# Kernel optimization log

Hardware: AMD Instinct MI355X
Metric: run time of the kernel (lower is better)

Reference implementation:

```python
import jax, jax.numpy as jnp
import numpy as np

UNITS = 512


def setup_inputs() -> dict:
    key = jax.random.key(0)
    ks = jax.random.split(key, 9)
    B, D, U = 16384, 512, UNITS
    return {
        "inputs": jax.random.normal(ks[0], (B, 2 * D), dtype=jnp.float32),
        "h": jax.random.normal(ks[1], (B, U), dtype=jnp.float32),
        "w_z": jax.random.normal(ks[2], (D, U), dtype=jnp.float32) * 0.05,
        "u_z": jax.random.normal(ks[3], (U, U), dtype=jnp.float32) * 0.05,
        "b_z": jnp.zeros((U,), dtype=jnp.float32),
        "w_r": jax.random.normal(ks[4], (D, U), dtype=jnp.float32) * 0.05,
        "u_r": jax.random.normal(ks[5], (U, U), dtype=jnp.float32) * 0.05,
        "b_r": jnp.zeros((U,), dtype=jnp.float32),
        "w_h": jax.random.normal(ks[6], (D, U), dtype=jnp.float32) * 0.05,
        "u_h": jax.random.normal(ks[7], (U, U), dtype=jnp.float32) * 0.05,
        "b_h": jnp.zeros((U,), dtype=jnp.float32),
    }


def reference(inputs, h, w_z, u_z, b_z, w_r, u_r, b_r, w_h, u_h, b_h):
    # Split concatenated (input, mask) halves along the feature axis.
    x, mask = jnp.split(inputs, 2, axis=1)  # each (B, D)
    # Faithful to source: mask @ zeros((D, U)) is identically zero.
    out_mask = jnp.matmul(mask, jnp.zeros((mask.shape[-1], UNITS), dtype=inputs.dtype))  # (B, U)
    h_masked = h * out_mask
    z_t = jax.nn.sigmoid(jnp.matmul(x, w_z) + jnp.matmul(h_masked, u_z) + b_z)
    r_t = jax.nn.sigmoid(jnp.matmul(x, w_r) + jnp.matmul(h_masked, u_r) + b_r)
    h_t = jnp.tanh(jnp.matmul(x, w_h) + jnp.matmul(r_t * h_masked, u_h) + b_h)
    h_t_seq = z_t * h_t + (1.0 - z_t) * h_masked  # (B, U)
    h_t_forward = jnp.concatenate((h_t_seq, out_mask), axis=1)  # (B, 2U)
    return (h_t_forward, h_t_seq)
```

## Files before the change

### kernel.cpp

```cpp
#include <hip/hip_runtime.h>

typedef __attribute__((ext_vector_type(4))) float f32x4;
typedef __attribute__((ext_vector_type(8))) short short8;
typedef __attribute__((ext_vector_type(8))) unsigned short ushort8;
typedef __attribute__((ext_vector_type(4))) unsigned short ushort4v;

#define M_ROWS 16384
#define KDIM 512
#define UDIM 512
#define IN_STRIDE 1024
#define NSTEP 16

__device__ __forceinline__ unsigned short f2bf(float f) {
    union { float f; unsigned u; } v; v.f = f;
    unsigned r = v.u + 0x7FFFu + ((v.u >> 16) & 1u);
    return (unsigned short)(r >> 16);
}

#define GLD16(g, l)                                                            \
    __builtin_amdgcn_global_load_lds(                                          \
        (const __attribute__((address_space(1))) void*)(g),                    \
        (__attribute__((address_space(3))) void*)(l), 16, 0, 0)

__global__ __launch_bounds__(256) void pack_w(
    const float* __restrict__ w_z,
    const float* __restrict__ w_h,
    unsigned short* __restrict__ Wp)
{
    int tid = blockIdx.x * 256 + threadIdx.x;
    int s   = tid & 511;
    int kt  = (tid >> 9) & 15;
    int ub  = tid >> 13;
    int jj  = s >> 2;
    int sl  = (s & 3) ^ ((jj >> 1) & 3);
    int k   = kt * 32 + sl * 8;
    const float* w = ((jj >> 5) & 1) ? w_h : w_z;
    int u = ub * 64 + ((jj >> 6) << 5) + (jj & 31);
    ushort8 v;
#pragma unroll
    for (int i = 0; i < 8; ++i)
        v[i] = f2bf(w[(size_t)(k + i) * UDIM + u]);
    *reinterpret_cast<ushort8*>(Wp + (size_t)tid * 8) = v;
}

__global__ __launch_bounds__(256, 3) void gru_gemm(
    const float* __restrict__ x,
    const unsigned short* __restrict__ Wp,
    const float* __restrict__ b_z,
    const float* __restrict__ b_h,
    float* __restrict__ out)
{
    __shared__ __align__(16) unsigned char smem[40960];
    unsigned short* shA = (unsigned short*)smem;
    unsigned short* shB = (unsigned short*)(smem + 16384);

    const int tid  = threadIdx.x;
    const int lane = tid & 63;
    const int wid  = tid >> 6;
    const int wm   = wid >> 1;
    const int wn   = wid & 1;

    const int d  = blockIdx.x;
    const int bx = (d >> 3) & 7;
    const int by = (d & 7) * 16 + (d >> 6);
    const int u0   = bx * 64;
    const int brow = by * 128;

    const int s0a = wid * 128 + lane;
    const int s1a = s0a + 64;
    const int r0 = s0a >> 2, r1 = s1a >> 2;
    const int sl0 = (s0a & 3) ^ ((r0 >> 1) & 3);
    const int sl1 = (s1a & 3) ^ ((r1 >> 1) & 3);
    const float* g0 = x + (size_t)(brow + r0) * IN_STRIDE + sl0 * 8;
    const float* g1 = x + (size_t)(brow + r1) * IN_STRIDE + sl1 * 8;

    const unsigned short* bp = Wp + (size_t)bx * 65536 + (size_t)s0a * 8;

    f32x4 acc[4][4];
#pragma unroll
    for (int m = 0; m < 4; ++m)
#pragma unroll
        for (int n = 0; n < 4; ++n)
            acc[m][n] = (f32x4){0.f, 0.f, 0.f, 0.f};

    f32x4 rA[2][4];

#define ISSUE_A(t, set)                                                        \
    {                                                                          \
        rA[set][0] = *reinterpret_cast<const f32x4*>(g0 + (t) * 32);           \
        rA[set][1] = *reinterpret_cast<const f32x4*>(g0 + (t) * 32 + 4);       \
        rA[set][2] = *reinterpret_cast<const f32x4*>(g1 + (t) * 32);           \
        rA[set][3] = *reinterpret_cast<const f32x4*>(g1 + (t) * 32 + 4);       \
    }

#define ISSUE_B(t, b)                                                          \
    {                                                                          \
        GLD16(bp + (size_t)(t) * 4096,       shB + (b) * 4096 + wid * 1024);   \
        GLD16(bp + (size_t)(t) * 4096 + 512, shB + (b) * 4096 + wid * 1024 + 512); \
    }

#define CVT_WRITE_A(set, b)                                                    \
    {                                                                          \
        ushort8 v0, v1;                                                        \
        _Pragma("unroll")                                                      \
        for (int i = 0; i < 4; ++i) { v0[i] = f2bf(rA[set][0][i]); v0[i+4] = f2bf(rA[set][1][i]); } \
        _Pragma("unroll")                                                      \
        for (int i = 0; i < 4; ++i) { v1[i] = f2bf(rA[set][2][i]); v1[i+4] = f2bf(rA[set][3][i]); } \
        *reinterpret_cast<ushort8*>(&shA[(b) * 4096 + s0a * 8]) = v0;          \
        *reinterpret_cast<ushort8*>(&shA[(b) * 4096 + s1a * 8]) = v1;          \
    }

    const int fr = lane & 15;
    const int ks = lane >> 4;
    const int xo = (fr >> 1) & 3;
    int aoff[4], boff[4];
#pragma unroll
    for (int m = 0; m < 4; ++m)
        aoff[m] = (wm * 64 + m * 16 + fr) * 32 + ((ks ^ xo) << 3);
#pragma unroll
    for (int n = 0; n < 4; ++n)
        boff[n] = (wn * 64 + n * 16 + fr) * 32 + ((ks ^ xo) << 3);

    ISSUE_A(0, 0); ISSUE_B(0, 0);
    ISSUE_A(1, 1); ISSUE_B(1, 1);
    asm volatile("s_waitcnt vmcnt(6)" ::: "memory");
    CVT_WRITE_A(0, 0);
    asm volatile("s_waitcnt lgkmcnt(0)" ::: "memory");
    asm volatile("s_barrier" ::: "memory");

#pragma unroll
    for (int t = 0; t < NSTEP; ++t) {
        if (t + 2 < NSTEP) {
            ISSUE_A(t + 2, (t + 2) & 1);
            ISSUE_B(t + 2, (t + 2) % 3);
        }
        const int ba = t & 1, bb = t % 3;
        short8 af[4], bfrag[4];
#pragma unroll
        for (int m = 0; m < 4; ++m)
            af[m] = *reinterpret_cast<const short8*>(&shA[ba * 4096 + aoff[m]]);
#pragma unroll
        for (int n = 0; n < 4; ++n)
            bfrag[n] = *reinterpret_cast<const short8*>(&shB[bb * 4096 + boff[n]]);
#pragma unroll
        for (int m = 0; m < 4; ++m)
#pragma unroll
            for (int n = 0; n < 4; ++n)
                acc[m][n] = __builtin_amdgcn_mfma_f32_16x16x32_bf16(af[m], bfrag[n], acc[m][n], 0, 0, 0);
        if (t + 1 < NSTEP) {
            if (t + 2 < NSTEP) {
                asm volatile("s_waitcnt vmcnt(6)" ::: "memory");
            } else {
                asm volatile("s_waitcnt vmcnt(0)" ::: "memory");
            }
            CVT_WRITE_A((t + 1) & 1, (t + 1) & 1);
            asm volatile("s_waitcnt lgkmcnt(0)" ::: "memory");
            asm volatile("s_barrier" ::: "memory");
        }
    }

    __syncthreads();

    float* plane = (float*)smem;
    const int fq = lane >> 4;
#pragma unroll
    for (int p = 0; p < 2; ++p) {
        int ucol = wn * 32 + p * 16 + fr;
        float bz = b_z[u0 + ucol];
        float bh = b_h[u0 + ucol];
#pragma unroll
        for (int m = 0; m < 4; ++m) {
            int row0 = wm * 64 + m * 16 + fq * 4;
            f32x4 az = acc[m][p];
            f32x4 ah = acc[m][p + 2];
#pragma unroll
            for (int j = 0; j < 4; ++j) {
                float zt = 1.f / (1.f + __expf(-(az[j] + bz)));
                float e  = __expf(2.f * (ah[j] + bh));
                float s  = zt * (1.f - 2.f / (e + 1.f));
                plane[(row0 + j) * 68 + ucol] = s;
            }
        }
    }
    __syncthreads();

    float* fwd = out;
    float* seq = out + (size_t)M_ROWS * 1024;
    const f32x4 z4 = (f32x4){0.f, 0.f, 0.f, 0.f};
    const int c4 = (tid & 15) * 4;
#pragma unroll
    for (int it = 0; it < 8; ++it) {
        int row = it * 16 + (tid >> 4);
        f32x4 v = *reinterpret_cast<const f32x4*>(&plane[row * 68 + c4]);
        size_t grow = (size_t)(brow + row);
        *reinterpret_cast<f32x4*>(&fwd[grow * 1024 + u0 + c4])       = v;
        *reinterpret_cast<f32x4*>(&fwd[grow * 1024 + 512 + u0 + c4]) = z4;
        *reinterpret_cast<f32x4*>(&seq[grow * 512 + u0 + c4])        = v;
    }
#undef ISSUE_A
#undef ISSUE_B
#undef CVT_WRITE_A
}

#define LDSS 40
__global__ __launch_bounds__(256) void gru_fused_legacy(
    const float* __restrict__ inp, const float* __restrict__ w_z,
    const float* __restrict__ b_z, const float* __restrict__ w_h,
    const float* __restrict__ b_h, float* __restrict__ out)
{
    __shared__ __align__(16) unsigned short Asl[2][128][LDSS];
    __shared__ __align__(16) unsigned short Bsl[2][128][LDSS];
    const int tid = threadIdx.x, lane = tid & 63, wid = tid >> 6;
    const int wm = wid >> 1, wn = wid & 1;
    const int u0 = blockIdx.x * 64, brow = blockIdx.y * 128;
    f32x4 acc[4][4];
#pragma unroll
    for (int m = 0; m < 4; ++m)
#pragma unroll
        for (int n = 0; n < 4; ++n) acc[m][n] = (f32x4){0.f,0.f,0.f,0.f};
    f32x4 rA[4], rB[4];
#define STAGE_LOAD(kt) { const int k0_=(kt)*32; \
    _Pragma("unroll") for (int it=0; it<4; ++it){ int idx=tid+256*it; int r=idx>>3,c=(idx&7)<<2; \
        rA[it]=*reinterpret_cast<const f32x4*>(inp+(size_t)(brow+r)*IN_STRIDE+k0_+c);} \
    _Pragma("unroll") for (int it=0; it<4; ++it){ int idx=tid+256*it; int jj=idx&127; int k4=(idx>>7)<<2; \
        const float* w_=((jj>>5)&1)?w_h:w_z; int u_=u0+((jj>>6)<<5)+(jj&31); \
        const float* p_=w_+(size_t)(k0_+k4)*UDIM+u_; \
        rB[it][0]=p_[0]; rB[it][1]=p_[UDIM]; rB[it][2]=p_[2*UDIM]; rB[it][3]=p_[3*UDIM];} }
#define STAGE_WRITE(bufi) { \
    _Pragma("unroll") for (int it=0; it<4; ++it){ int idx=tid+256*it; int r=idx>>3,c=(idx&7)<<2; ushort4v v; \
        v[0]=f2bf(rA[it][0]); v[1]=f2bf(rA[it][1]); v[2]=f2bf(rA[it][2]); v[3]=f2bf(rA[it][3]); \
        *reinterpret_cast<ushort4v*>(&Asl[bufi][r][c])=v;} \
    _Pragma("unroll") for (int it=0; it<4; ++it){ int idx=tid+256*it; int jj=idx&127; int k4=(idx>>7)<<2; ushort4v v; \
        v[0]=f2bf(rB[it][0]); v[1]=f2bf(rB[it][1]); v[2]=f2bf(rB[it][2]); v[3]=f2bf(rB[it][3]); \
        *reinterpret_cast<ushort4v*>(&Bsl[bufi][jj][k4])=v;} }
    STAGE_LOAD(0); STAGE_WRITE(0);
    const int fr = lane & 15, koff = (lane >> 4) << 3;
    for (int kt = 0; kt < NSTEP; ++kt) {
        if (kt + 1 < NSTEP) STAGE_LOAD(kt + 1);
        __syncthreads();
        const int buf = kt & 1;
        short8 af[4], bfr[4];
#pragma unroll
        for (int m = 0; m < 4; ++m) af[m] = *reinterpret_cast<const short8*>(&Asl[buf][wm*64+m*16+fr][koff]);
#pragma unroll
        for (int n = 0; n < 4; ++n) bfr[n] = *reinterpret_cast<const short8*>(&Bsl[buf][wn*64+n*16+fr][koff]);
#pragma unroll
        for (int m = 0; m < 4; ++m)
#pragma unroll
            for (int n = 0; n < 4; ++n)
                acc[m][n] = __builtin_amdgcn_mfma_f32_16x16x32_bf16(af[m], bfr[n], acc[m][n], 0, 0, 0);
        if (kt + 1 < NSTEP) STAGE_WRITE((kt + 1) & 1);
    }
    float* fwd = out; float* seq = out + (size_t)M_ROWS * 1024;
    const int fq = lane >> 4;
#pragma unroll
    for (int p = 0; p < 2; ++p) {
        int u = u0 + wn * 32 + p * 16 + fr;
        float bz = b_z[u], bh = b_h[u];
#pragma unroll
        for (int m = 0; m < 4; ++m) {
            int row0 = brow + wm * 64 + m * 16 + fq * 4;
            f32x4 az = acc[m][p], ah = acc[m][p + 2];
#pragma unroll
            for (int j = 0; j < 4; ++j) {
                float zt = 1.f / (1.f + __expf(-(az[j] + bz)));
                float e  = __expf(2.f * (ah[j] + bh));
                float s  = zt * (1.f - 2.f / (e + 1.f));
                size_t rr = (size_t)(row0 + j);
                fwd[rr * 1024 + u] = s;
                fwd[rr * 1024 + 512 + u] = 0.f;
                seq[rr * 512 + u] = s;
            }
        }
    }
}

extern "C" void kernel_launch(void* const* d_in, const int* in_sizes, int n_in,
                              void* d_out, int out_size, void* d_ws, size_t ws_size,
                              hipStream_t stream) {
    const float* inp = (const float*)d_in[0];
    const float* w_z = (const float*)d_in[2];
    const float* b_z = (const float*)d_in[4];
    const float* w_h = (const float*)d_in[8];
    const float* b_h = (const float*)d_in[10];
    float* out = (float*)d_out;

    const size_t needW = (size_t)8 * 16 * 512 * 16;
    if (ws_size >= needW) {
        unsigned short* Wp = (unsigned short*)d_ws;
        hipLaunchKernelGGL(pack_w, dim3(256), dim3(256), 0, stream, w_z, w_h, Wp);
        hipLaunchKernelGGL(gru_gemm, dim3(1024), dim3(256), 0, stream,
                           inp, Wp, b_z, b_h, out);
    } else {
        hipLaunchKernelGGL(gru_fused_legacy, dim3(8, 128), dim3(256), 0, stream,
                           inp, w_z, b_z, w_h, b_h, out);
    }
}
```

Measured before the change: 52.05 us.

## Load GEMM operands directly into registers, drop LDS staging, offload zero-fill

```diff
diff --git a/kernel.cpp b/kernel.cpp
--- a/kernel.cpp
+++ b/kernel.cpp
@@ -17,42 +17,46 @@
     return (unsigned short)(r >> 16);
 }
 
-#define GLD16(g, l)                                                            \
-    __builtin_amdgcn_global_load_lds(                                          \
-        (const __attribute__((address_space(1))) void*)(g),                    \
-        (__attribute__((address_space(3))) void*)(l), 16, 0, 0)
-
-__global__ __launch_bounds__(256) void pack_w(
+__global__ __launch_bounds__(256) void pack_and_zero(
     const float* __restrict__ w_z,
     const float* __restrict__ w_h,
-    unsigned short* __restrict__ Wp)
+    unsigned short* __restrict__ Wp,
+    float* __restrict__ out)
 {
-    int tid = blockIdx.x * 256 + threadIdx.x;
-    int s   = tid & 511;
-    int kt  = (tid >> 9) & 15;
-    int ub  = tid >> 13;
-    int jj  = s >> 2;
-    int sl  = (s & 3) ^ ((jj >> 1) & 3);
-    int k   = kt * 32 + sl * 8;
-    const float* w = ((jj >> 5) & 1) ? w_h : w_z;
-    int u = ub * 64 + ((jj >> 6) << 5) + (jj & 31);
-    ushort8 v;
-#pragma unroll
-    for (int i = 0; i < 8; ++i)
-        v[i] = f2bf(w[(size_t)(k + i) * UDIM + u]);
-    *reinterpret_cast<ushort8*>(Wp + (size_t)tid * 8) = v;
-}
-
-__global__ __launch_bounds__(256, 3) void gru_gemm(
+    const int bid = blockIdx.x;
+    if (bid < 256) {
+        int tid = bid * 256 + threadIdx.x;
+        int ub  = tid >> 13;
+        int t   = (tid >> 9) & 15;
+        int s   = tid & 511;
+        int jj  = s >> 2;
+        int ks  = s & 3;
+        int k   = t * 32 + ks * 8;
+        const float* w = ((jj >> 5) & 1) ? w_h : w_z;
+        int u = ub * 64 + ((jj >> 6) << 5) + (jj & 31);
+        ushort8 v;
+#pragma unroll
+        for (int i = 0; i < 8; ++i)
+            v[i] = f2bf(w[(size_t)(k + i) * UDIM + u]);
+        *reinterpret_cast<ushort8*>(Wp + (size_t)tid * 8) = v;
+    } else {
+        int g   = (bid - 256) * 256 + threadIdx.x;
+        int row = g >> 7;
+        int c4  = (g & 127) << 2;
+        const f32x4 z4 = (f32x4){0.f, 0.f, 0.f, 0.f};
+        __builtin_nontemporal_store(
+            z4, reinterpret_cast<f32x4*>(out + (size_t)row * 1024 + 512 + c4));
+    }
+}
+
+__global__ __launch_bounds__(256, 2) void gru_gemm(
     const float* __restrict__ x,
     const unsigned short* __restrict__ Wp,
     const float* __restrict__ b_z,
     const float* __restrict__ b_h,
     float* __restrict__ out)
 {
-    __shared__ __align__(16) unsigned char smem[40960];
-    unsigned short* shA = (unsigned short*)smem;
-    unsigned short* shB = (unsigned short*)(smem + 16384);
+    __shared__ __align__(16) float plane[128 * 68];
 
     const int tid  = threadIdx.x;
     const int lane = tid & 63;
@@ -66,15 +70,18 @@
     const int u0   = bx * 64;
     const int brow = by * 128;
 
-    const int s0a = wid * 128 + lane;
-    const int s1a = s0a + 64;
-    const int r0 = s0a >> 2, r1 = s1a >> 2;
-    const int sl0 = (s0a & 3) ^ ((r0 >> 1) & 3);
-    const int sl1 = (s1a & 3) ^ ((r1 >> 1) & 3);
-    const float* g0 = x + (size_t)(brow + r0) * IN_STRIDE + sl0 * 8;
-    const float* g1 = x + (size_t)(brow + r1) * IN_STRIDE + sl1 * 8;
-
-    const unsigned short* bp = Wp + (size_t)bx * 65536 + (size_t)s0a * 8;
+    const int fr = lane & 15;
+    const int ks = lane >> 4;
+
+    const float* gA[4];
+#pragma unroll
+    for (int m = 0; m < 4; ++m)
+        gA[m] = x + (size_t)(brow + wm * 64 + m * 16 + fr) * IN_STRIDE + ks * 8;
+    const unsigned short* gB[4];
+#pragma unroll
+    for (int n = 0; n < 4; ++n)
+        gB[n] = Wp + (size_t)bx * 65536
+                   + (size_t)(((wn * 64 + n * 16 + fr) << 2) + ks) * 8;
 
     f32x4 acc[4][4];
 #pragma unroll
@@ -83,86 +90,46 @@
         for (int n = 0; n < 4; ++n)
             acc[m][n] = (f32x4){0.f, 0.f, 0.f, 0.f};
 
-    f32x4 rA[2][4];
-
-#define ISSUE_A(t, set)                                                        \
+    f32x4 lo[2][4], hi[2][4];
+    short8 rb[2][4];
+
+#define ISSUE(t, st)                                                           \
     {                                                                          \
-        rA[set][0] = *reinterpret_cast<const f32x4*>(g0 + (t) * 32);           \
-        rA[set][1] = *reinterpret_cast<const f32x4*>(g0 + (t) * 32 + 4);       \
-        rA[set][2] = *reinterpret_cast<const f32x4*>(g1 + (t) * 32);           \
-        rA[set][3] = *reinterpret_cast<const f32x4*>(g1 + (t) * 32 + 4);       \
-    }
-
-#define ISSUE_B(t, b)                                                          \
-    {                                                                          \
-        GLD16(bp + (size_t)(t) * 4096,       shB + (b) * 4096 + wid * 1024);   \
-        GLD16(bp + (size_t)(t) * 4096 + 512, shB + (b) * 4096 + wid * 1024 + 512); \
-    }
-
-#define CVT_WRITE_A(set, b)                                                    \
-    {                                                                          \
-        ushort8 v0, v1;                                                        \
         _Pragma("unroll")                                                      \
-        for (int i = 0; i < 4; ++i) { v0[i] = f2bf(rA[set][0][i]); v0[i+4] = f2bf(rA[set][1][i]); } \
+        for (int m = 0; m < 4; ++m) {                                          \
+            lo[st][m] = *reinterpret_cast<const f32x4*>(gA[m] + (t) * 32);     \
+            hi[st][m] = *reinterpret_cast<const f32x4*>(gA[m] + (t) * 32 + 4); \
+        }                                                                      \
         _Pragma("unroll")                                                      \
-        for (int i = 0; i < 4; ++i) { v1[i] = f2bf(rA[set][2][i]); v1[i+4] = f2bf(rA[set][3][i]); } \
-        *reinterpret_cast<ushort8*>(&shA[(b) * 4096 + s0a * 8]) = v0;          \
-        *reinterpret_cast<ushort8*>(&shA[(b) * 4096 + s1a * 8]) = v1;          \
-    }
-
-    const int fr = lane & 15;
-    const int ks = lane >> 4;
-    const int xo = (fr >> 1) & 3;
-    int aoff[4], boff[4];
-#pragma unroll
-    for (int m = 0; m < 4; ++m)
-        aoff[m] = (wm * 64 + m * 16 + fr) * 32 + ((ks ^ xo) << 3);
-#pragma unroll
-    for (int n = 0; n < 4; ++n)
-        boff[n] = (wn * 64 + n * 16 + fr) * 32 + ((ks ^ xo) << 3);
-
-    ISSUE_A(0, 0); ISSUE_B(0, 0);
-    ISSUE_A(1, 1); ISSUE_B(1, 1);
-    asm volatile("s_waitcnt vmcnt(6)" ::: "memory");
-    CVT_WRITE_A(0, 0);
-    asm volatile("s_waitcnt lgkmcnt(0)" ::: "memory");
-    asm volatile("s_barrier" ::: "memory");
+        for (int n = 0; n < 4; ++n)                                            \
+            rb[st][n] = *reinterpret_cast<const short8*>(gB[n] + (size_t)(t) * 4096); \
+    }
+
+    ISSUE(0, 0);
 
 #pragma unroll
     for (int t = 0; t < NSTEP; ++t) {
-        if (t + 2 < NSTEP) {
-            ISSUE_A(t + 2, (t + 2) & 1);
-            ISSUE_B(t + 2, (t + 2) % 3);
+        if (t + 1 < NSTEP) ISSUE(t + 1, (t + 1) & 1);
+        const int st = t & 1;
+        short8 af[4];
+#pragma unroll
+        for (int m = 0; m < 4; ++m) {
+#pragma unroll
+            for (int i = 0; i < 4; ++i) {
+                af[m][i]     = (short)f2bf(lo[st][m][i]);
+                af[m][4 + i] = (short)f2bf(hi[st][m][i]);
+            }
         }
-        const int ba = t & 1, bb = t % 3;
-        short8 af[4], bfrag[4];
 #pragma unroll
         for (int m = 0; m < 4; ++m)
-            af[m] = *reinterpret_cast<const short8*>(&shA[ba * 4096 + aoff[m]]);
-#pragma unroll
-        for (int n = 0; n < 4; ++n)
-            bfrag[n] = *reinterpret_cast<const short8*>(&shB[bb * 4096 + boff[n]]);
-#pragma unroll
-        for (int m = 0; m < 4; ++m)
 #pragma unroll
             for (int n = 0; n < 4; ++n)
-                acc[m][n] = __builtin_amdgcn_mfma_f32_16x16x32_bf16(af[m], bfrag[n], acc[m][n], 0, 0, 0);
-        if (t + 1 < NSTEP) {
-            if (t + 2 < NSTEP) {
-                asm volatile("s_waitcnt vmcnt(6)" ::: "memory");
-            } else {
-                asm volatile("s_waitcnt vmcnt(0)" ::: "memory");
-            }
-            CVT_WRITE_A((t + 1) & 1, (t + 1) & 1);
-            asm volatile("s_waitcnt lgkmcnt(0)" ::: "memory");
-            asm volatile("s_barrier" ::: "memory");
-        }
-    }
-
-    __syncthreads();
-
-    float* plane = (float*)smem;
-    const int fq = lane >> 4;
+                acc[m][n] = __builtin_amdgcn_mfma_f32_16x16x32_bf16(
+                    af[m], rb[st][n], acc[m][n], 0, 0, 0);
+    }
+#undef ISSUE
+
+    const int fq = ks;
 #pragma unroll
     for (int p = 0; p < 2; ++p) {
         int ucol = wn * 32 + p * 16 + fr;
@@ -186,20 +153,17 @@
 
     float* fwd = out;
     float* seq = out + (size_t)M_ROWS * 1024;
-    const f32x4 z4 = (f32x4){0.f, 0.f, 0.f, 0.f};
     const int c4 = (tid & 15) * 4;
 #pragma unroll
     for (int it = 0; it < 8; ++it) {
         int row = it * 16 + (tid >> 4);
         f32x4 v = *reinterpret_cast<const f32x4*>(&plane[row * 68 + c4]);
         size_t grow = (size_t)(brow + row);
-        *reinterpret_cast<f32x4*>(&fwd[grow * 1024 + u0 + c4])       = v;
-        *reinterpret_cast<f32x4*>(&fwd[grow * 1024 + 512 + u0 + c4]) = z4;
-        *reinterpret_cast<f32x4*>(&seq[grow * 512 + u0 + c4])        = v;
-    }
-#undef ISSUE_A
-#undef ISSUE_B
-#undef CVT_WRITE_A
+        __builtin_nontemporal_store(
+            v, reinterpret_cast<f32x4*>(&fwd[grow * 1024 + u0 + c4]));
+        __builtin_nontemporal_store(
+            v, reinterpret_cast<f32x4*>(&seq[grow * 512 + u0 + c4]));
+    }
 }
 
 #define LDSS 40
@@ -288,7 +252,8 @@
     const size_t needW = (size_t)8 * 16 * 512 * 16;
     if (ws_size >= needW) {
         unsigned short* Wp = (unsigned short*)d_ws;
-        hipLaunchKernelGGL(pack_w, dim3(256), dim3(256), 0, stream, w_z, w_h, Wp);
+        hipLaunchKernelGGL(pack_and_zero, dim3(256 + 8192), dim3(256), 0, stream,
+                           w_z, w_h, Wp, out);
         hipLaunchKernelGGL(gru_gemm, dim3(1024), dim3(256), 0, stream,
                            inp, Wp, b_z, b_h, out);
     } else {
```

Result: slower. 98.92 us (+90.1%).

## Double the GEMM K-step to 64 with new swizzled LDS layout

Applied to the files above, without the earlier changes.

```diff
diff --git a/kernel.cpp b/kernel.cpp
--- a/kernel.cpp
+++ b/kernel.cpp
@@ -1,4 +1,5 @@
 #include <hip/hip_runtime.h>
+#include <hip/hip_bf16.h>
 
 typedef __attribute__((ext_vector_type(4))) float f32x4;
 typedef __attribute__((ext_vector_type(8))) short short8;
@@ -9,12 +10,17 @@
 #define KDIM 512
 #define UDIM 512
 #define IN_STRIDE 1024
-#define NSTEP 16
+#define NPH 8
 
 __device__ __forceinline__ unsigned short f2bf(float f) {
     union { float f; unsigned u; } v; v.f = f;
     unsigned r = v.u + 0x7FFFu + ((v.u >> 16) & 1u);
     return (unsigned short)(r >> 16);
+}
+
+__device__ __forceinline__ unsigned cvt2(float a, float b) {
+    __hip_bfloat162 h = __float22bfloat162_rn(float2{a, b});
+    union { __hip_bfloat162 h; unsigned u; } c; c.h = h; return c.u;
 }
 
 #define GLD16(g, l)                                                            \
@@ -27,32 +33,33 @@
     const float* __restrict__ w_h,
     unsigned short* __restrict__ Wp)
 {
-    int tid = blockIdx.x * 256 + threadIdx.x;
-    int s   = tid & 511;
-    int kt  = (tid >> 9) & 15;
-    int ub  = tid >> 13;
-    int jj  = s >> 2;
-    int sl  = (s & 3) ^ ((jj >> 1) & 3);
-    int k   = kt * 32 + sl * 8;
+    int g  = blockIdx.x * 256 + threadIdx.x;
+    int S  = g & 1023;
+    int ph = (g >> 10) & 7;
+    int ub = g >> 13;
+    int jj = S >> 3;
+    int P  = S & 7;
+    int L  = P ^ (jj & 7);
+    int k0 = ph * 64 + L * 8;
     const float* w = ((jj >> 5) & 1) ? w_h : w_z;
     int u = ub * 64 + ((jj >> 6) << 5) + (jj & 31);
     ushort8 v;
 #pragma unroll
     for (int i = 0; i < 8; ++i)
-        v[i] = f2bf(w[(size_t)(k + i) * UDIM + u]);
-    *reinterpret_cast<ushort8*>(Wp + (size_t)tid * 8) = v;
-}
-
-__global__ __launch_bounds__(256, 3) void gru_gemm(
+        v[i] = f2bf(w[(size_t)(k0 + i) * UDIM + u]);
+    *reinterpret_cast<ushort8*>(Wp + (size_t)g * 8) = v;
+}
+
+__global__ __launch_bounds__(256, 2) void gru_gemm(
     const float* __restrict__ x,
     const unsigned short* __restrict__ Wp,
     const float* __restrict__ b_z,
     const float* __restrict__ b_h,
     float* __restrict__ out)
 {
-    __shared__ __align__(16) unsigned char smem[40960];
+    __shared__ __align__(16) unsigned char smem[81920];
     unsigned short* shA = (unsigned short*)smem;
-    unsigned short* shB = (unsigned short*)(smem + 16384);
+    unsigned short* shB = (unsigned short*)(smem + 32768);
 
     const int tid  = threadIdx.x;
     const int lane = tid & 63;
@@ -66,15 +73,13 @@
     const int u0   = bx * 64;
     const int brow = by * 128;
 
-    const int s0a = wid * 128 + lane;
-    const int s1a = s0a + 64;
-    const int r0 = s0a >> 2, r1 = s1a >> 2;
-    const int sl0 = (s0a & 3) ^ ((r0 >> 1) & 3);
-    const int sl1 = (s1a & 3) ^ ((r1 >> 1) & 3);
-    const float* g0 = x + (size_t)(brow + r0) * IN_STRIDE + sl0 * 8;
-    const float* g1 = x + (size_t)(brow + r1) * IN_STRIDE + sl1 * 8;
-
-    const unsigned short* bp = Wp + (size_t)bx * 65536 + (size_t)s0a * 8;
+    const int rrow = tid & 127;
+    const int rs   = tid >> 7;
+    const float* gAr = x + (size_t)(brow + rrow) * IN_STRIDE + rs * 32;
+    const int awbase = rrow * 64;
+    const int rx7    = rrow & 7;
+
+    const unsigned short* bp = Wp + (size_t)bx * 65536;
 
     f32x4 acc[4][4];
 #pragma unroll
@@ -83,77 +88,89 @@
         for (int n = 0; n < 4; ++n)
             acc[m][n] = (f32x4){0.f, 0.f, 0.f, 0.f};
 
-    f32x4 rA[2][4];
-
-#define ISSUE_A(t, set)                                                        \
+    f32x4 rA[8];
+
+#define ISSUE_A(ph)                                                            \
     {                                                                          \
-        rA[set][0] = *reinterpret_cast<const f32x4*>(g0 + (t) * 32);           \
-        rA[set][1] = *reinterpret_cast<const f32x4*>(g0 + (t) * 32 + 4);       \
-        rA[set][2] = *reinterpret_cast<const f32x4*>(g1 + (t) * 32);           \
-        rA[set][3] = *reinterpret_cast<const f32x4*>(g1 + (t) * 32 + 4);       \
-    }
-
-#define ISSUE_B(t, b)                                                          \
+        _Pragma("unroll")                                                      \
+        for (int i = 0; i < 8; ++i)                                            \
+            rA[i] = *reinterpret_cast<const f32x4*>(gAr + (ph) * 64 + i * 4);  \
+    }
+
+#define ISSUE_B(ph, b)                                                         \
     {                                                                          \
-        GLD16(bp + (size_t)(t) * 4096,       shB + (b) * 4096 + wid * 1024);   \
-        GLD16(bp + (size_t)(t) * 4096 + 512, shB + (b) * 4096 + wid * 1024 + 512); \
-    }
-
-#define CVT_WRITE_A(set, b)                                                    \
+        _Pragma("unroll")                                                      \
+        for (int i = 0; i < 4; ++i)                                            \
+            GLD16(bp + (size_t)(ph) * 8192 + (wid * 256 + i * 64 + lane) * 8,  \
+                  shB + (b) * 8192 + wid * 2048 + i * 512);                    \
+    }
+
+#define CVT_WRITE_A(ph)                                                        \
     {                                                                          \
-        ushort8 v0, v1;                                                        \
+        const int ab_ = ((ph) & 1) * 8192;                                     \
         _Pragma("unroll")                                                      \
-        for (int i = 0; i < 4; ++i) { v0[i] = f2bf(rA[set][0][i]); v0[i+4] = f2bf(rA[set][1][i]); } \
-        _Pragma("unroll")                                                      \
-        for (int i = 0; i < 4; ++i) { v1[i] = f2bf(rA[set][2][i]); v1[i+4] = f2bf(rA[set][3][i]); } \
-        *reinterpret_cast<ushort8*>(&shA[(b) * 4096 + s0a * 8]) = v0;          \
-        *reinterpret_cast<ushort8*>(&shA[(b) * 4096 + s1a * 8]) = v1;          \
-    }
-
-    const int fr = lane & 15;
-    const int ks = lane >> 4;
-    const int xo = (fr >> 1) & 3;
-    int aoff[4], boff[4];
+        for (int j = 0; j < 4; ++j) {                                          \
+            union { unsigned u[4]; ushort8 v; } c;                             \
+            c.u[0] = cvt2(rA[2 * j][0], rA[2 * j][1]);                         \
+            c.u[1] = cvt2(rA[2 * j][2], rA[2 * j][3]);                         \
+            c.u[2] = cvt2(rA[2 * j + 1][0], rA[2 * j + 1][1]);                 \
+            c.u[3] = cvt2(rA[2 * j + 1][2], rA[2 * j + 1][3]);                 \
+            int piece = (rs * 4 + j) ^ rx7;                                    \
+            *reinterpret_cast<ushort8*>(&shA[ab_ + awbase + piece * 8]) = c.v; \
+        }                                                                      \
+    }
+
+    const int fr  = lane & 15;
+    const int ks  = lane >> 4;
+    const int pc0 = (ks)     ^ (fr & 7);
+    const int pc1 = (4 + ks) ^ (fr & 7);
+    int arow[4], brw[4];
 #pragma unroll
     for (int m = 0; m < 4; ++m)
-        aoff[m] = (wm * 64 + m * 16 + fr) * 32 + ((ks ^ xo) << 3);
+        arow[m] = (wm * 64 + m * 16 + fr) * 64;
 #pragma unroll
     for (int n = 0; n < 4; ++n)
-        boff[n] = (wn * 64 + n * 16 + fr) * 32 + ((ks ^ xo) << 3);
-
-    ISSUE_A(0, 0); ISSUE_B(0, 0);
-    ISSUE_A(1, 1); ISSUE_B(1, 1);
-    asm volatile("s_waitcnt vmcnt(6)" ::: "memory");
-    CVT_WRITE_A(0, 0);
+        brw[n] = (wn * 64 + n * 16 + fr) * 64;
+
+    ISSUE_A(0);
+    ISSUE_B(0, 0);
+    ISSUE_B(1, 1);
+    asm volatile("s_waitcnt vmcnt(4)" ::: "memory");
+    CVT_WRITE_A(0);
     asm volatile("s_waitcnt lgkmcnt(0)" ::: "memory");
     asm volatile("s_barrier" ::: "memory");
 
 #pragma unroll
-    for (int t = 0; t < NSTEP; ++t) {
-        if (t + 2 < NSTEP) {
-            ISSUE_A(t + 2, (t + 2) & 1);
-            ISSUE_B(t + 2, (t + 2) % 3);
-        }
-        const int ba = t & 1, bb = t % 3;
-        short8 af[4], bfrag[4];
+    for (int p = 0; p < NPH; ++p) {
+        if (p + 1 < NPH) ISSUE_A(p + 1);
+        if (p + 2 < NPH) ISSUE_B(p + 2, (p + 2) % 3);
+        const int ab = (p & 1) * 8192;
+        const int bb = (p % 3) * 8192;
+        short8 af0[4], af1[4], bf0[4], bf1[4];
+#pragma unroll
+        for (int m = 0; m < 4; ++m) {
+            af0[m] = *reinterpret_cast<const short8*>(&shA[ab + arow[m] + pc0 * 8]);
+            af1[m] = *reinterpret_cast<const short8*>(&shA[ab + arow[m] + pc1 * 8]);
+        }
+#pragma unroll
+        for (int n = 0; n < 4; ++n) {
+            bf0[n] = *reinterpret_cast<const short8*>(&shB[bb + brw[n] + pc0 * 8]);
+            bf1[n] = *reinterpret_cast<const short8*>(&shB[bb + brw[n] + pc1 * 8]);
+        }
 #pragma unroll
         for (int m = 0; m < 4; ++m)
-            af[m] = *reinterpret_cast<const short8*>(&shA[ba * 4096 + aoff[m]]);
-#pragma unroll
-        for (int n = 0; n < 4; ++n)
-            bfrag[n] = *reinterpret_cast<const short8*>(&shB[bb * 4096 + boff[n]]);
-#pragma unroll
-        for (int m = 0; m < 4; ++m)
-#pragma unroll
-            for (int n = 0; n < 4; ++n)
-                acc[m][n] = __builtin_amdgcn_mfma_f32_16x16x32_bf16(af[m], bfrag[n], acc[m][n], 0, 0, 0);
-        if (t + 1 < NSTEP) {
-            if (t + 2 < NSTEP) {
-                asm volatile("s_waitcnt vmcnt(6)" ::: "memory");
+#pragma unroll
+            for (int n = 0; n < 4; ++n) {
+                acc[m][n] = __builtin_amdgcn_mfma_f32_16x16x32_bf16(af0[m], bf0[n], acc[m][n], 0, 0, 0);
+                acc[m][n] = __builtin_amdgcn_mfma_f32_16x16x32_bf16(af1[m], bf1[n], acc[m][n], 0, 0, 0);
+            }
+        if (p + 1 < NPH) {
+            if (p + 2 < NPH) {
+                asm volatile("s_waitcnt vmcnt(4)" ::: "memory");
             } else {
                 asm volatile("s_waitcnt vmcnt(0)" ::: "memory");
             }
-            CVT_WRITE_A((t + 1) & 1, (t + 1) & 1);
+            CVT_WRITE_A(p + 1);
             asm volatile("s_waitcnt lgkmcnt(0)" ::: "memory");
             asm volatile("s_barrier" ::: "memory");
         }
@@ -162,7 +179,7 @@
     __syncthreads();
 
     float* plane = (float*)smem;
-    const int fq = lane >> 4;
+    const int fq = ks;
 #pragma unroll
     for (int p = 0; p < 2; ++p) {
         int ucol = wn * 32 + p * 16 + fr;
@@ -203,6 +220,7 @@
 }
 
 #define LDSS 40
+#define NSTEP 16
 __global__ __launch_bounds__(256) void gru_fused_legacy(
     const float* __restrict__ inp, const float* __restrict__ w_z,
     const float* __restrict__ b_z, const float* __restrict__ w_h,
@@ -285,7 +303,7 @@
     const float* b_h = (const float*)d_in[10];
     float* out = (float*)d_out;
 
-    const size_t needW = (size_t)8 * 16 * 512 * 16;
+    const size_t needW = (size_t)8 * 8 * 1024 * 16;
     if (ws_size >= needW) {
         unsigned short* Wp = (unsigned short*)d_ws;
         hipLaunchKernelGGL(pack_w, dim3(256), dim3(256), 0, stream, w_z, w_h, Wp);
```

Result: slower. 64.63 us (+24.2%).
